# Kernel optimization log

Measured on AMD Instinct MI355X. Metric: run time of the kernel, lower is better.

## Reference

```python
import jax, jax.numpy as jnp
import numpy as np

N_NODES = 100000


def _graph_conv(x, W, b, src, dst, n_nodes):
    # dgl GraphConv, norm='both'. in_dim >= out_dim so weight is applied first.
    E = src.shape[0]
    ones = jnp.ones((E,), dtype=x.dtype)
    deg_out = jnp.clip(jax.ops.segment_sum(ones, src, num_segments=n_nodes), 1.0)
    deg_in = jnp.clip(jax.ops.segment_sum(ones, dst, num_segments=n_nodes), 1.0)
    h = x @ W                                  # [N, out]
    h = h * (deg_out ** -0.5)[:, None]          # src-side norm D_out^{-1/2}
    agg = jax.ops.segment_sum(h[src], dst, num_segments=n_nodes)  # SpMM
    agg = agg * (deg_in ** -0.5)[:, None]       # dst-side norm D_in^{-1/2}
    return agg + b


def setup_inputs() -> dict:
    key = jax.random.key(0)
    k1, k2, k3, k4, k5, k6, k7 = jax.random.split(key, 7)
    in_dim, hidden_dim, out_dim = 256, 128, 40
    E = 3200000
    h = jax.random.normal(k1, (N_NODES, in_dim), dtype=jnp.float32)
    src = jax.random.randint(k2, (E,), 0, N_NODES)
    dst = jax.random.randint(k3, (E,), 0, N_NODES)
    # Glorot-style init for GraphConv weights, zero bias (dgl default)
    W1 = jax.random.normal(k4, (in_dim, hidden_dim), dtype=jnp.float32) / np.sqrt(in_dim)
    b1 = jnp.zeros((hidden_dim,), dtype=jnp.float32)
    W2 = jax.random.normal(k5, (hidden_dim, out_dim), dtype=jnp.float32) / np.sqrt(hidden_dim)
    b2 = jnp.zeros((out_dim,), dtype=jnp.float32)
    return {"h": h, "W1": W1, "b1": b1, "W2": W2, "b2": b2, "src": src, "dst": dst}


def reference(h, W1, b1, W2, b2, src, dst):
    n = h.shape[0]
    # CRD: GraphConv -> relu (dropout is identity in eval)
    x = _graph_conv(h, W1, b1, src, dst, n)
    x = jax.nn.relu(x)
    # CLS: GraphConv -> log_softmax over classes
    x = _graph_conv(x, W2, b2, src, dst, n)
    return jax.nn.log_softmax(x, axis=1)
```

## Files before the change

kernel.cpp:

```cpp
#include <hip/hip_runtime.h>
#include <hip/hip_bf16.h>
#include <cstddef>
#include <cstdint>

#define IN_DIM 256
#define HID 128
#define OUT_DIM 40

#define CHUNK 8192
#define BIN_SHIFT 10
#define BIN_SIZE 1024
#define MAXB 128
#define GSPLIT 8

typedef __attribute__((ext_vector_type(8))) short short8;
typedef __attribute__((ext_vector_type(4))) float f32x4;
typedef __attribute__((ext_vector_type(2))) float f32x2;

__device__ inline short f2bf(float f) {
    __hip_bfloat16 b = __float2bfloat16(f);
    return __builtin_bit_cast(short, b);
}
__device__ inline float bf2f(unsigned short u) {
    unsigned int v = (unsigned int)u << 16;
    return __builtin_bit_cast(float, v);
}
__device__ inline int permf(int p) { return (p >> 3) + 16 * (p & 7); }

__global__ __launch_bounds__(256) void k_setup(const float* __restrict__ W1, const float* __restrict__ W2,
                                               const float* __restrict__ b1, short* __restrict__ Wg,
                                               short* __restrict__ Wg2, float* __restrict__ b1p,
                                               int* __restrict__ deg_in, int* __restrict__ deg_out, int Z) {
    int flat = blockIdx.x * 256 + threadIdx.x;
    if (flat < 8192) {
        int k = flat >> 5;
        int n0 = (flat & 31) * 4;
        float4 v = *(const float4*)(W1 + (size_t)k * HID + n0);
        int ks = k >> 5, quad = (k >> 3) & 3, j = k & 7;
        float vv[4] = {v.x, v.y, v.z, v.w};
#pragma unroll
        for (int e = 0; e < 4; ++e) {
            int n = n0 + e;
            int nt = n >> 4;
            int ln = (n & 15) | (quad << 4);
            Wg[(((nt * 8 + ks) * 64) + ln) * 8 + j] = f2bf(vv[e]);
        }
        return;
    }
    flat -= 8192;
    if (flat < 3 * 4 * 64 * 8) {
        int f = flat >> 9;
        int ln = (flat >> 3) & 63;
        int j = flat & 7;
        int nt = f >> 2, ks = f & 3;
        int q = ks * 32 + (ln >> 4) * 8 + j;
        int c = nt * 16 + (ln & 15);
        float v = (c < OUT_DIM) ? W2[(size_t)permf(q) * OUT_DIM + c] : 0.f;
        Wg2[flat] = f2bf(v);
        return;
    }
    flat -= 3 * 4 * 64 * 8;
    if (flat < HID) { b1p[flat] = b1[permf(flat)]; return; }
    flat -= HID;
    if (flat < Z) { *(int4*)(deg_in + flat * 4) = make_int4(0, 0, 0, 0); return; }
    flat -= Z;
    if (flat < Z) { *(int4*)(deg_out + flat * 4) = make_int4(0, 0, 0, 0); }
}

__global__ __launch_bounds__(256) void k_binscatter(const int* __restrict__ src, const int* __restrict__ dst,
                                                    uint32_t* __restrict__ stD, unsigned short* __restrict__ stS,
                                                    int* __restrict__ bboD, int* __restrict__ bboS,
                                                    int E, int NBINS) {
    __shared__ int hD[MAXB], hS[MAXB], cD[MAXB], cS[MAXB], sd[MAXB];
    int j = blockIdx.x, t = threadIdx.x;
    int base = j * CHUNK;
    int nE = min(CHUNK, E - base);
    int NB1 = NBINS + 1;
    for (int i = t; i < MAXB; i += 256) { hD[i] = 0; hS[i] = 0; }
    __syncthreads();
    for (int i = t; i < nE; i += 256) {
        atomicAdd(&hD[dst[base + i] >> BIN_SHIFT], 1);
        atomicAdd(&hS[src[base + i] >> BIN_SHIFT], 1);
    }
    __syncthreads();
    if (t < MAXB) sd[t] = hD[t];
    __syncthreads();
    for (int off = 1; off < MAXB; off <<= 1) {
        int x = 0;
        if (t < MAXB && t >= off) x = sd[t - off];
        __syncthreads();
        if (t < MAXB) sd[t] += x;
        __syncthreads();
    }
    if (t < MAXB) cD[t] = sd[t] - hD[t];
    if (t < NBINS) bboD[(size_t)j * NB1 + t] = sd[t] - hD[t];
    if (t == NBINS) bboD[(size_t)j * NB1 + NBINS] = nE;
    __syncthreads();
    if (t < MAXB) sd[t] = hS[t];
    __syncthreads();
    for (int off = 1; off < MAXB; off <<= 1) {
        int x = 0;
        if (t < MAXB && t >= off) x = sd[t - off];
        __syncthreads();
        if (t < MAXB) sd[t] += x;
        __syncthreads();
    }
    if (t < MAXB) cS[t] = sd[t] - hS[t];
    if (t < NBINS) bboS[(size_t)j * NB1 + t] = sd[t] - hS[t];
    if (t == NBINS) bboS[(size_t)j * NB1 + NBINS] = nE;
    __syncthreads();
    for (int i = t; i < nE; i += 256) {
        int s = src[base + i], d = dst[base + i];
        int pD = atomicAdd(&cD[d >> BIN_SHIFT], 1);
        stD[(size_t)base + pD] = ((uint32_t)(d & (BIN_SIZE - 1)) << 17) | (uint32_t)s;
        int pS = atomicAdd(&cS[s >> BIN_SHIFT], 1);
        stS[(size_t)base + pS] = (unsigned short)(s & (BIN_SIZE - 1));
    }
}

__global__ __launch_bounds__(256) void k_deg(const uint32_t* __restrict__ stD, const int* __restrict__ bboD,
                                             const unsigned short* __restrict__ stS, const int* __restrict__ bboS,
                                             int* __restrict__ deg_in, int* __restrict__ deg_out,
                                             int* __restrict__ hsave, int nchunk, int NBINS) {
    __shared__ int hist[BIN_SIZE];
    int b = blockIdx.x, g = blockIdx.y, t = threadIdx.x;
    int wv = t >> 6, lane = t & 63;
    int NB1 = NBINS + 1;
    for (int i = t; i < BIN_SIZE; i += 256) hist[i] = 0;
    __syncthreads();
    int base = b << BIN_SHIFT;
    if (blockIdx.z == 0) {
        for (int j = g * 4 + wv; j < nchunk; j += GSPLIT * 4) {
            int s = bboD[(size_t)j * NB1 + b], e = bboD[(size_t)j * NB1 + b + 1];
            const uint32_t* seg = stD + (size_t)j * CHUNK;
            for (int i = s + lane; i < e; i += 64)
                atomicAdd(&hist[seg[i] >> 17], 1);
        }
        __syncthreads();
        int* hp = hsave + ((size_t)(b * GSPLIT + g) << BIN_SHIFT);
        for (int i = t; i < BIN_SIZE; i += 256) {
            int v = hist[i];
            hp[i] = v;
            if (v) atomicAdd(&deg_in[base + i], v);
        }
    } else {
        for (int j = g * 4 + wv; j < nchunk; j += GSPLIT * 4) {
            int s = bboS[(size_t)j * NB1 + b], e = bboS[(size_t)j * NB1 + b + 1];
            const unsigned short* seg = stS + (size_t)j * CHUNK;
            for (int i = s + lane; i < e; i += 64)
                atomicAdd(&hist[seg[i]], 1);
        }
        __syncthreads();
        for (int i = t; i < BIN_SIZE; i += 256) {
            int v = hist[i];
            if (v) atomicAdd(&deg_out[base + i], v);
        }
    }
}

__global__ __launch_bounds__(256) void k_col(const uint32_t* __restrict__ stD, const int* __restrict__ bboD,
                                             const int* __restrict__ hsave, int* __restrict__ cursor,
                                             int* __restrict__ col, int N, int nchunk, int NBINS) {
    __shared__ int hist[BIN_SIZE];
    int b = blockIdx.x, g = blockIdx.y, t = threadIdx.x;
    int wv = t >> 6, lane = t & 63;
    int NB1 = NBINS + 1;
    int base = b << BIN_SHIFT;
    const int* hp = hsave + ((size_t)(b * GSPLIT + g) << BIN_SHIFT);
    for (int i = t; i < BIN_SIZE; i += 256) {
        int v = hp[i];
        hist[i] = v ? atomicAdd(&cursor[base + i], v) : 0;
    }
    __syncthreads();
    for (int j = g * 4 + wv; j < nchunk; j += GSPLIT * 4) {
        int s = bboD[(size_t)j * NB1 + b], e = bboD[(size_t)j * NB1 + b + 1];
        const uint32_t* seg = stD + (size_t)j * CHUNK;
        for (int i = s + lane; i < e; i += 64) {
            uint32_t v = seg[i];
            int pos = atomicAdd(&hist[v >> 17], 1);
            col[pos] = (int)(v & 0x1FFFFu);
        }
    }
}

__global__ __launch_bounds__(256) void k_scan1(const int* __restrict__ deg, int* __restrict__ out,
                                               int* __restrict__ bsum, float* __restrict__ rs_in, int n) {
    __shared__ int sd[256];
    int t = threadIdx.x, b = blockIdx.x;
    int base = b * 1024 + t * 4;
    int v0 = 0, v1 = 0, v2 = 0, v3 = 0;
    if (base + 0 < n) v0 = deg[base + 0];
    if (base + 1 < n) v1 = deg[base + 1];
    if (base + 2 < n) v2 = deg[base + 2];
    if (base + 3 < n) v3 = deg[base + 3];
    if (base + 0 < n) rs_in[base + 0] = rsqrtf((float)max(v0, 1));
    if (base + 1 < n) rs_in[base + 1] = rsqrtf((float)max(v1, 1));
    if (base + 2 < n) rs_in[base + 2] = rsqrtf((float)max(v2, 1));
    if (base + 3 < n) rs_in[base + 3] = rsqrtf((float)max(v3, 1));
    int ts = v0 + v1 + v2 + v3;
    sd[t] = ts;
    __syncthreads();
    for (int off = 1; off < 256; off <<= 1) {
        int x = 0;
        if (t >= off) x = sd[t - off];
        __syncthreads();
        sd[t] += x;
        __syncthreads();
    }
    int excl = sd[t] - ts;
    if (base + 0 < n) out[base + 0] = excl;
    if (base + 1 < n) out[base + 1] = excl + v0;
    if (base + 2 < n) out[base + 2] = excl + v0 + v1;
    if (base + 3 < n) out[base + 3] = excl + v0 + v1 + v2;
    if (t == 255) bsum[b] = sd[255];
}

__global__ __launch_bounds__(1024) void k_scan2(int* __restrict__ bsum, int nb) {
    __shared__ int sd[1024];
    int t = threadIdx.x;
    int v = (t < nb) ? bsum[t] : 0;
    sd[t] = v;
    __syncthreads();
    for (int off = 1; off < 1024; off <<= 1) {
        int x = 0;
        if (t >= off) x = sd[t - off];
        __syncthreads();
        sd[t] += x;
        __syncthreads();
    }
    if (t < nb) bsum[t] = sd[t] - v;
}

__global__ __launch_bounds__(256) void k_scan3(int* __restrict__ row_ptr, const int* __restrict__ bsum,
                                               int* __restrict__ cursor, const int* __restrict__ deg_out,
                                               float* __restrict__ rs_out, int n, int E) {
    int i = blockIdx.x * 256 + threadIdx.x;
    if (i < n) {
        int v = row_ptr[i] + bsum[i >> 10];
        row_ptr[i] = v;
        cursor[i] = v;
        rs_out[i] = rsqrtf((float)max(deg_out[i], 1));
    }
    if (i == 0) row_ptr[n] = E;
}

__global__ __launch_bounds__(256) void k_gemm1(const float* __restrict__ A, const short* __restrict__ Wg,
                                               const float* __restrict__ rs_out, uint32_t* __restrict__ h1f, int M) {
    __shared__ short As[64 * 264];
    int t = threadIdx.x;
    int lane = t & 63, wv = t >> 6;
    int block_row = blockIdx.x * 64;
#pragma unroll
    for (int i = 0; i < 16; ++i) {
        int u = t + i * 256;
        int row = u >> 6, kq = (u & 63) * 4;
        int gr = block_row + row;
        float4 v = {0.f, 0.f, 0.f, 0.f};
        if (gr < M) v = *(const float4*)(A + (size_t)gr * IN_DIM + kq);
        short4 sv = {f2bf(v.x), f2bf(v.y), f2bf(v.z), f2bf(v.w)};
        *(short4*)&As[row * 264 + kq] = sv;
    }
    __syncthreads();
    f32x4 acc[8] = {};
    int arow = (wv * 16 + (lane & 15)) * 264 + (lane >> 4) * 8;
#pragma unroll
    for (int ks = 0; ks < 8; ++ks) {
        short8 a = *(short8*)&As[arow + ks * 32];
#pragma unroll
        for (int nt = 0; nt < 8; ++nt) {
            short8 b = *(const short8*)&Wg[(((nt * 8 + ks) * 64) + lane) * 8];
            acc[nt] = __builtin_amdgcn_mfma_f32_16x16x32_bf16(a, b, acc[nt], 0, 0, 0);
        }
    }
    int quad = lane >> 4, cl = lane & 15;
#pragma unroll
    for (int r = 0; r < 4; ++r) {
        int gr = block_row + wv * 16 + quad * 4 + r;
        if (gr >= M) continue;
        float sc = rs_out[gr];
        int d0 = __builtin_amdgcn_cvt_pk_fp8_f32(acc[0][r] * sc, acc[1][r] * sc, 0, false);
        d0 = __builtin_amdgcn_cvt_pk_fp8_f32(acc[2][r] * sc, acc[3][r] * sc, d0, true);
        int d1 = __builtin_amdgcn_cvt_pk_fp8_f32(acc[4][r] * sc, acc[5][r] * sc, 0, false);
        d1 = __builtin_amdgcn_cvt_pk_fp8_f32(acc[6][r] * sc, acc[7][r] * sc, d1, true);
        uint2 dd = make_uint2((uint32_t)d0, (uint32_t)d1);
        *(uint2*)((char*)h1f + (size_t)gr * 128 + cl * 8) = dd;
    }
}

__global__ __launch_bounds__(256) void k_spmm1f(const char* __restrict__ h1c, const int* __restrict__ rp,
                                                const int* __restrict__ col, const float* __restrict__ rs_in,
                                                const float* __restrict__ rs_out, const float* __restrict__ b1p,
                                                const short* __restrict__ Wg2,
                                                uint32_t* __restrict__ h2f, int N) {
    __shared__ uint32_t x1s[16 * 64];
    __shared__ uint32_t hs2[48];
    int t = threadIdx.x;
    int wv = t >> 6, lane = t & 63;
    int grp = lane >> 4, ql = lane & 15;
    int w_base = blockIdx.x * 4;
    int w = w_base + wv;

    float4 blo = *(const float4*)&b1p[ql * 8];
    float4 bhi = *(const float4*)&b1p[ql * 8 + 4];

    if (w < N) {
        int s = rp[w], e = rp[w + 1];
        f32x2 a0 = {0.f, 0.f}, a1 = {0.f, 0.f}, a2 = {0.f, 0.f}, a3 = {0.f, 0.f};
        int qoff = ql << 3;
        int i = s;
        while (i < e) {
            int cnt = min(64, e - i);
            int cl = (lane < cnt) ? lane : cnt - 1;
            int rof = col[i + cl] << 7;
            int nfull = cnt & ~15;
            int it = 0;
            for (; it < nfull; it += 16) {
                int o0 = __shfl(rof, it + grp, 64) + qoff;
                int o1 = __shfl(rof, it + 4 + grp, 64) + qoff;
                int o2 = __shfl(rof, it + 8 + grp, 64) + qoff;
                int o3 = __shfl(rof, it + 12 + grp, 64) + qoff;
                uint2 u0 = *(const uint2*)(h1c + (uint32_t)o0);
                uint2 u1 = *(const uint2*)(h1c + (uint32_t)o1);
                uint2 u2 = *(const uint2*)(h1c + (uint32_t)o2);
                uint2 u3 = *(const uint2*)(h1c + (uint32_t)o3);
                a0 += __builtin_amdgcn_cvt_pk_f32_fp8(u0.x, false);
                a1 += __builtin_amdgcn_cvt_pk_f32_fp8(u0.x, true);
                a2 += __builtin_amdgcn_cvt_pk_f32_fp8(u0.y, false);
                a3 += __builtin_amdgcn_cvt_pk_f32_fp8(u0.y, true);
                a0 += __builtin_amdgcn_cvt_pk_f32_fp8(u1.x, false);
                a1 += __builtin_amdgcn_cvt_pk_f32_fp8(u1.x, true);
                a2 += __builtin_amdgcn_cvt_pk_f32_fp8(u1.y, false);
                a3 += __builtin_amdgcn_cvt_pk_f32_fp8(u1.y, true);
                a0 += __builtin_amdgcn_cvt_pk_f32_fp8(u2.x, false);
                a1 += __builtin_amdgcn_cvt_pk_f32_fp8(u2.x, true);
                a2 += __builtin_amdgcn_cvt_pk_f32_fp8(u2.y, false);
                a3 += __builtin_amdgcn_cvt_pk_f32_fp8(u2.y, true);
                a0 += __builtin_amdgcn_cvt_pk_f32_fp8(u3.x, false);
                a1 += __builtin_amdgcn_cvt_pk_f32_fp8(u3.x, true);
                a2 += __builtin_amdgcn_cvt_pk_f32_fp8(u3.y, false);
                a3 += __builtin_amdgcn_cvt_pk_f32_fp8(u3.y, true);
            }
            if (it < cnt) {
                int e0 = it + grp;
                int o0 = __shfl(rof, e0, 64) + qoff;
                int o1 = __shfl(rof, e0 + 4, 64) + qoff;
                int o2 = __shfl(rof, e0 + 8, 64) + qoff;
                int o3 = __shfl(rof, e0 + 12, 64) + qoff;
                float mv0 = (e0 < cnt) ? 1.f : 0.f;
                float mv1 = (e0 + 4 < cnt) ? 1.f : 0.f;
                float mv2 = (e0 + 8 < cnt) ? 1.f : 0.f;
                float mv3 = (e0 + 12 < cnt) ? 1.f : 0.f;
                f32x2 m0 = {mv0, mv0}, m1 = {mv1, mv1}, m2 = {mv2, mv2}, m3 = {mv3, mv3};
                uint2 u0 = *(const uint2*)(h1c + (uint32_t)o0);
                uint2 u1 = *(const uint2*)(h1c + (uint32_t)o1);
                uint2 u2 = *(const uint2*)(h1c + (uint32_t)o2);
                uint2 u3 = *(const uint2*)(h1c + (uint32_t)o3);
                a0 += __builtin_amdgcn_cvt_pk_f32_fp8(u0.x, false) * m0;
                a1 += __builtin_amdgcn_cvt_pk_f32_fp8(u0.x, true) * m0;
                a2 += __builtin_amdgcn_cvt_pk_f32_fp8(u0.y, false) * m0;
                a3 += __builtin_amdgcn_cvt_pk_f32_fp8(u0.y, true) * m0;
                a0 += __builtin_amdgcn_cvt_pk_f32_fp8(u1.x, false) * m1;
                a1 += __builtin_amdgcn_cvt_pk_f32_fp8(u1.x, true) * m1;
                a2 += __builtin_amdgcn_cvt_pk_f32_fp8(u1.y, false) * m1;
                a3 += __builtin_amdgcn_cvt_pk_f32_fp8(u1.y, true) * m1;
                a0 += __builtin_amdgcn_cvt_pk_f32_fp8(u2.x, false) * m2;
                a1 += __builtin_amdgcn_cvt_pk_f32_fp8(u2.x, true) * m2;
                a2 += __builtin_amdgcn_cvt_pk_f32_fp8(u2.y, false) * m2;
                a3 += __builtin_amdgcn_cvt_pk_f32_fp8(u2.y, true) * m2;
                a0 += __builtin_amdgcn_cvt_pk_f32_fp8(u3.x, false) * m3;
                a1 += __builtin_amdgcn_cvt_pk_f32_fp8(u3.x, true) * m3;
                a2 += __builtin_amdgcn_cvt_pk_f32_fp8(u3.y, false) * m3;
                a3 += __builtin_amdgcn_cvt_pk_f32_fp8(u3.y, true) * m3;
            }
            i += cnt;
        }
        float ac[8] = {a0.x, a0.y, a1.x, a1.y, a2.x, a2.y, a3.x, a3.y};
#pragma unroll
        for (int j = 0; j < 8; ++j) {
            ac[j] += __shfl_xor(ac[j], 16, 64);
            ac[j] += __shfl_xor(ac[j], 32, 64);
        }
        if (lane < 16) {
            float sc = rs_in[w];
            float f0, f1;
            uint32_t o0, o1, o2, o3;
            f0 = fmaxf(fmaf(ac[0], sc, blo.x), 0.f); f1 = fmaxf(fmaf(ac[1], sc, blo.y), 0.f);
            o0 = (uint32_t)(unsigned short)f2bf(f0) | ((uint32_t)(unsigned short)f2bf(f1) << 16);
            f0 = fmaxf(fmaf(ac[2], sc, blo.z), 0.f); f1 = fmaxf(fmaf(ac[3], sc, blo.w), 0.f);
            o1 = (uint32_t)(unsigned short)f2bf(f0) | ((uint32_t)(unsigned short)f2bf(f1) << 16);
            f0 = fmaxf(fmaf(ac[4], sc, bhi.x), 0.f); f1 = fmaxf(fmaf(ac[5], sc, bhi.y), 0.f);
            o2 = (uint32_t)(unsigned short)f2bf(f0) | ((uint32_t)(unsigned short)f2bf(f1) << 16);
            f0 = fmaxf(fmaf(ac[6], sc, bhi.z), 0.f); f1 = fmaxf(fmaf(ac[7], sc, bhi.w), 0.f);
            o3 = (uint32_t)(unsigned short)f2bf(f0) | ((uint32_t)(unsigned short)f2bf(f1) << 16);
            int woff = (wv * 256 + ql * 16) ^ ((wv & 7) << 4);
            *(uint4*)((char*)x1s + woff) = make_uint4(o0, o1, o2, o3);
        }
    }
    __syncthreads();
    int vr = min(4, N - w_base);
    if (wv < 3) {
        short8 wf0 = *(const short8*)&Wg2[((wv * 4 + 0) * 64 + lane) * 8];
        short8 wf1 = *(const short8*)&Wg2[((wv * 4 + 1) * 64 + lane) * 8];
        short8 wf2 = *(const short8*)&Wg2[((wv * 4 + 2) * 64 + lane) * 8];
        short8 wf3 = *(const short8*)&Wg2[((wv * 4 + 3) * 64 + lane) * 8];
        int row = lane & 15, kc = lane >> 4;
        int rbase = row * 256 + kc * 16;
        int swz = (row & 7) << 4;
        f32x4 c = {};
        c = __builtin_amdgcn_mfma_f32_16x16x32_bf16(*(short8*)((char*)x1s + ((rbase + 0) ^ swz)),   wf0, c, 0, 0, 0);
        c = __builtin_amdgcn_mfma_f32_16x16x32_bf16(*(short8*)((char*)x1s + ((rbase + 64) ^ swz)),  wf1, c, 0, 0, 0);
        c = __builtin_amdgcn_mfma_f32_16x16x32_bf16(*(short8*)((char*)x1s + ((rbase + 128) ^ swz)), wf2, c, 0, 0, 0);
        c = __builtin_amdgcn_mfma_f32_16x16x32_bf16(*(short8*)((char*)x1s + ((rbase + 192) ^ swz)), wf3, c, 0, 0, 0);
        int cc = wv * 16 + row;
        if (cc < OUT_DIM && kc == 0) {
            float s0 = rs_out[w_base + 0];
            float s1 = (vr > 1) ? rs_out[w_base + 1] : 0.f;
            float s2 = (vr > 2) ? rs_out[w_base + 2] : 0.f;
            float s3 = (vr > 3) ? rs_out[w_base + 3] : 0.f;
            int pk = __builtin_amdgcn_cvt_pk_fp8_f32(c[0] * s0, c[1] * s1, 0, false);
            pk = __builtin_amdgcn_cvt_pk_fp8_f32(c[2] * s2, c[3] * s3, pk, true);
            hs2[cc] = (uint32_t)pk;
        }
    }
    __syncthreads();
    if (t < 64) {
        int node = t >> 4, d = t & 15;
        uint32_t v = 0;
        if (d < 10) {
            int sh = node * 8;
            uint32_t b0 = (hs2[4 * d + 0] >> sh) & 0xffu;
            uint32_t b1 = (hs2[4 * d + 1] >> sh) & 0xffu;
            uint32_t b2 = (hs2[4 * d + 2] >> sh) & 0xffu;
            uint32_t b3 = (hs2[4 * d + 3] >> sh) & 0xffu;
            v = b0 | (b1 << 8) | (b2 << 16) | (b3 << 24);
        }
        if (node < vr) h2f[(size_t)(w_base + node) * 16 + d] = v;
    }
}

__global__ __launch_bounds__(256) void k_spmm2(const char* __restrict__ h2c, const int* __restrict__ rp,
                                               const int* __restrict__ col, const float* __restrict__ rs_in,
                                               const float* __restrict__ b2, float* __restrict__ out, int n) {
    int w = (blockIdx.x * 256 + threadIdx.x) >> 6;
    int lane = threadIdx.x & 63;
    if (w >= n) return;
    int grp = lane >> 3, fl = lane & 7;
    int qoff = fl << 3;
    int s = rp[w], e = rp[w + 1];
    f32x2 a0 = {0.f, 0.f}, a1 = {0.f, 0.f}, a2 = {0.f, 0.f}, a3 = {0.f, 0.f};
    int i = s;
    while (i < e) {
        int cnt = min(64, e - i);
        int cl = (lane < cnt) ? lane : cnt - 1;
        int rof = col[i + cl] << 6;
        int nfull = cnt & ~31;
        int it = 0;
        for (; it < nfull; it += 32) {
            int o0 = __shfl(rof, it + grp, 64) + qoff;
            int o1 = __shfl(rof, it + 8 + grp, 64) + qoff;
            int o2 = __shfl(rof, it + 16 + grp, 64) + qoff;
            int o3 = __shfl(rof, it + 24 + grp, 64) + qoff;
            uint2 u0 = *(const uint2*)(h2c + (uint32_t)o0);
            uint2 u1 = *(const uint2*)(h2c + (uint32_t)o1);
            uint2 u2 = *(const uint2*)(h2c + (uint32_t)o2);
            uint2 u3 = *(const uint2*)(h2c + (uint32_t)o3);
            a0 += __builtin_amdgcn_cvt_pk_f32_fp8(u0.x, false);
            a1 += __builtin_amdgcn_cvt_pk_f32_fp8(u0.x, true);
            a2 += __builtin_amdgcn_cvt_pk_f32_fp8(u0.y, false);
            a3 += __builtin_amdgcn_cvt_pk_f32_fp8(u0.y, true);
            a0 += __builtin_amdgcn_cvt_pk_f32_fp8(u1.x, false);
            a1 += __builtin_amdgcn_cvt_pk_f32_fp8(u1.x, true);
            a2 += __builtin_amdgcn_cvt_pk_f32_fp8(u1.y, false);
            a3 += __builtin_amdgcn_cvt_pk_f32_fp8(u1.y, true);
            a0 += __builtin_amdgcn_cvt_pk_f32_fp8(u2.x, false);
            a1 += __builtin_amdgcn_cvt_pk_f32_fp8(u2.x, true);
            a2 += __builtin_amdgcn_cvt_pk_f32_fp8(u2.y, false);
            a3 += __builtin_amdgcn_cvt_pk_f32_fp8(u2.y, true);
            a0 += __builtin_amdgcn_cvt_pk_f32_fp8(u3.x, false);
            a1 += __builtin_amdgcn_cvt_pk_f32_fp8(u3.x, true);
            a2 += __builtin_amdgcn_cvt_pk_f32_fp8(u3.y, false);
            a3 += __builtin_amdgcn_cvt_pk_f32_fp8(u3.y, true);
        }
        if (it < cnt) {
            int e0 = it + grp;
            int o0 = __shfl(rof, e0, 64) + qoff;
            int o1 = __shfl(rof, e0 + 8, 64) + qoff;
            int o2 = __shfl(rof, e0 + 16, 64) + qoff;
            int o3 = __shfl(rof, e0 + 24, 64) + qoff;
            float mv0 = (e0 < cnt) ? 1.f : 0.f;
            float mv1 = (e0 + 8 < cnt) ? 1.f : 0.f;
            float mv2 = (e0 + 16 < cnt) ? 1.f : 0.f;
            float mv3 = (e0 + 24 < cnt) ? 1.f : 0.f;
            f32x2 m0 = {mv0, mv0}, m1 = {mv1, mv1}, m2 = {mv2, mv2}, m3 = {mv3, mv3};
            uint2 u0 = *(const uint2*)(h2c + (uint32_t)o0);
            uint2 u1 = *(const uint2*)(h2c + (uint32_t)o1);
            uint2 u2 = *(const uint2*)(h2c + (uint32_t)o2);
            uint2 u3 = *(const uint2*)(h2c + (uint32_t)o3);
            a0 += __builtin_amdgcn_cvt_pk_f32_fp8(u0.x, false) * m0;
            a1 += __builtin_amdgcn_cvt_pk_f32_fp8(u0.x, true) * m0;
            a2 += __builtin_amdgcn_cvt_pk_f32_fp8(u0.y, false) * m0;
            a3 += __builtin_amdgcn_cvt_pk_f32_fp8(u0.y, true) * m0;
            a0 += __builtin_amdgcn_cvt_pk_f32_fp8(u1.x, false) * m1;
            a1 += __builtin_amdgcn_cvt_pk_f32_fp8(u1.x, true) * m1;
            a2 += __builtin_amdgcn_cvt_pk_f32_fp8(u1.y, false) * m1;
            a3 += __builtin_amdgcn_cvt_pk_f32_fp8(u1.y, true) * m1;
            a0 += __builtin_amdgcn_cvt_pk_f32_fp8(u2.x, false) * m2;
            a1 += __builtin_amdgcn_cvt_pk_f32_fp8(u2.x, true) * m2;
            a2 += __builtin_amdgcn_cvt_pk_f32_fp8(u2.y, false) * m2;
            a3 += __builtin_amdgcn_cvt_pk_f32_fp8(u2.y, true) * m2;
            a0 += __builtin_amdgcn_cvt_pk_f32_fp8(u3.x, false) * m3;
            a1 += __builtin_amdgcn_cvt_pk_f32_fp8(u3.x, true) * m3;
            a2 += __builtin_amdgcn_cvt_pk_f32_fp8(u3.y, false) * m3;
            a3 += __builtin_amdgcn_cvt_pk_f32_fp8(u3.y, true) * m3;
        }
        i += cnt;
    }
    float ac[8] = {a0.x, a0.y, a1.x, a1.y, a2.x, a2.y, a3.x, a3.y};
#pragma unroll
    for (int j = 0; j < 8; ++j) {
        ac[j] += __shfl_xor(ac[j], 8, 64);
        ac[j] += __shfl_xor(ac[j], 16, 64);
        ac[j] += __shfl_xor(ac[j], 32, 64);
    }
    bool act = lane < 5;
    float sc = rs_in[w];
    int bb = (fl < 5) ? fl * 8 : 0;
    float val[8];
#pragma unroll
    for (int j = 0; j < 8; ++j)
        val[j] = fmaf(ac[j], sc, b2[bb + j]);
    float pm = -INFINITY;
    if (act) {
        pm = val[0];
#pragma unroll
        for (int j = 1; j < 8; ++j) pm = fmaxf(pm, val[j]);
    }
    pm = fmaxf(pm, __shfl_xor(pm, 4, 8));
    pm = fmaxf(pm, __shfl_xor(pm, 2, 8));
    pm = fmaxf(pm, __shfl_xor(pm, 1, 8));
    float ex = 0.f;
    if (act) {
#pragma unroll
        for (int j = 0; j < 8; ++j) ex += expf(val[j] - pm);
    }
    ex += __shfl_xor(ex, 4, 8);
    ex += __shfl_xor(ex, 2, 8);
    ex += __shfl_xor(ex, 1, 8);
    if (act) {
        float l = pm + logf(ex);
        float4 o0 = {val[0] - l, val[1] - l, val[2] - l, val[3] - l};
        float4 o1 = {val[4] - l, val[5] - l, val[6] - l, val[7] - l};
        float* op = out + (size_t)w * OUT_DIM + lane * 8;
        *(float4*)op = o0;
        *(float4*)(op + 4) = o1;
    }
}


extern "C" void kernel_launch(void* const* d_in, const int* in_sizes, int n_in,
                              void* d_out, int out_size, void* d_ws, size_t ws_size,
                              hipStream_t stream) {
    const int N = in_sizes[0] / IN_DIM;
    const int E = in_sizes[5];
    const float* h  = (const float*)d_in[0];
    const float* W1 = (const float*)d_in[1];
    const float* b1 = (const float*)d_in[2];
    const float* W2 = (const float*)d_in[3];
    const float* b2 = (const float*)d_in[4];
    const int* src  = (const int*)d_in[5];
    const int* dst  = (const int*)d_in[6];
    float* out = (float*)d_out;

    const int NBINS  = (N + BIN_SIZE - 1) >> BIN_SHIFT;
    const int NCHUNK = (E + CHUNK - 1) / CHUNK;

    char* w = (char*)d_ws;
    size_t off = 0;
    auto alloc = [&](size_t bytes) -> void* {
        void* p = w + off;
        off += (bytes + 255) & ~(size_t)255;
        return p;
    };
    int* deg_in   = (int*)alloc((size_t)N * 4);
    int* deg_out  = (int*)alloc((size_t)N * 4);
    int* row_ptr  = (int*)alloc((size_t)(N + 1) * 4);
    int* cursor   = (int*)alloc((size_t)N * 4);
    int* bsum     = (int*)alloc(1024 * 4);
    float* rs_out = (float*)alloc((size_t)N * 4);
    float* rs_in  = (float*)alloc((size_t)N * 4);
    int* col      = (int*)alloc((size_t)E * 4);
    int* bboD     = (int*)alloc((size_t)NCHUNK * (NBINS + 1) * 4);
    int* bboS     = (int*)alloc((size_t)NCHUNK * (NBINS + 1) * 4);
    short* Wg     = (short*)alloc((size_t)8 * 8 * 64 * 8 * 2);
    short* Wg2    = (short*)alloc((size_t)3 * 4 * 64 * 8 * 2);
    float* b1p    = (float*)alloc((size_t)HID * 4);
    int* hsave    = (int*)alloc((size_t)NBINS * GSPLIT * BIN_SIZE * 4);
    size_t stD_bytes = (size_t)E * 4;  if ((size_t)N * HID > stD_bytes) stD_bytes = (size_t)N * HID;
    size_t stS_bytes = (size_t)E * 2;  if ((size_t)N * 64 > stS_bytes) stS_bytes = (size_t)N * 64;
    uint32_t* stD = (uint32_t*)alloc(stD_bytes);
    unsigned short* stS = (unsigned short*)alloc(stS_bytes);
    uint32_t* h1f = (uint32_t*)stD;
    uint32_t* h2f = (uint32_t*)stS;

    int gN = (N + 255) / 256;
    int NB = (N + 1023) / 1024;
    int Z = (N + 3) / 4;
    int setup_units = 8192 + 3 * 4 * 64 * 8 + HID + 2 * Z;
    int gsetup = (setup_units + 255) / 256;

    k_setup<<<gsetup, 256, 0, stream>>>(W1, W2, b1, Wg, Wg2, b1p, deg_in, deg_out, Z);
    k_binscatter<<<NCHUNK, 256, 0, stream>>>(src, dst, stD, stS, bboD, bboS, E, NBINS);
    k_deg<<<dim3(NBINS, GSPLIT, 2), 256, 0, stream>>>(stD, bboD, stS, bboS, deg_in, deg_out, hsave, NCHUNK, NBINS);
    k_scan1<<<NB, 256, 0, stream>>>(deg_in, row_ptr, bsum, rs_in, N);
    k_scan2<<<1, 1024, 0, stream>>>(bsum, NB);
    k_scan3<<<gN, 256, 0, stream>>>(row_ptr, bsum, cursor, deg_out, rs_out, N, E);
    k_col<<<dim3(NBINS, GSPLIT), 256, 0, stream>>>(stD, bboD, hsave, cursor, col, N, NCHUNK, NBINS);
    k_gemm1<<<(N + 63) / 64, 256, 0, stream>>>(h, Wg, rs_out, h1f, N);
    k_spmm1f<<<(N + 3) / 4, 256, 0, stream>>>((const char*)h1f, row_ptr, col, rs_in, rs_out, b1p, Wg2, h2f, N);
    k_spmm2<<<(N + 3) / 4, 256, 0, stream>>>((const char*)h2f, row_ptr, col, rs_in, b2, out, N);
}
```

Before: 463.1 us.

## Stage binned edges in shared memory, halve chunk size, fold block-sum scan into scan3

The bin-scatter kernel now writes binned edges into shared-memory staging arrays and then copies them to global memory with coalesced vector stores, replacing scattered global writes. The chunk size is halved to 4096 edges, which keeps the staging buffers within shared memory and doubles the number of blocks. The separate single-block scan2 launch is removed; each scan3 block redundantly scans up to 128 block sums itself. The trade-offs are more per-chunk offset metadata, which k_deg and k_col must then read, a redundant small scan in every scan3 block, and the assumption that NB is at most 128.

```diff
diff --git a/kernel.cpp b/kernel.cpp
--- a/kernel.cpp
+++ b/kernel.cpp
@@ -7,7 +7,7 @@
 #define HID 128
 #define OUT_DIM 40
 
-#define CHUNK 8192
+#define CHUNK 4096
 #define BIN_SHIFT 10
 #define BIN_SIZE 1024
 #define MAXB 128
@@ -71,7 +71,9 @@
                                                     uint32_t* __restrict__ stD, unsigned short* __restrict__ stS,
                                                     int* __restrict__ bboD, int* __restrict__ bboS,
                                                     int E, int NBINS) {
-    __shared__ int hD[MAXB], hS[MAXB], cD[MAXB], cS[MAXB], sd[MAXB];
+    __shared__ __align__(16) uint32_t sgD[CHUNK];
+    __shared__ __align__(16) unsigned short sgS[CHUNK];
+    __shared__ int hD[MAXB], hS[MAXB], sd[MAXB];
     int j = blockIdx.x, t = threadIdx.x;
     int base = j * CHUNK;
     int nE = min(CHUNK, E - base);
@@ -92,8 +94,12 @@
         if (t < MAXB) sd[t] += x;
         __syncthreads();
     }
-    if (t < MAXB) cD[t] = sd[t] - hD[t];
-    if (t < NBINS) bboD[(size_t)j * NB1 + t] = sd[t] - hD[t];
+    if (t < MAXB) {
+        int h = hD[t];
+        int c = sd[t] - h;
+        hD[t] = c;
+        if (t < NBINS) bboD[(size_t)j * NB1 + t] = c;
+    }
     if (t == NBINS) bboD[(size_t)j * NB1 + NBINS] = nE;
     __syncthreads();
     if (t < MAXB) sd[t] = hS[t];
@@ -105,17 +111,30 @@
         if (t < MAXB) sd[t] += x;
         __syncthreads();
     }
-    if (t < MAXB) cS[t] = sd[t] - hS[t];
-    if (t < NBINS) bboS[(size_t)j * NB1 + t] = sd[t] - hS[t];
+    if (t < MAXB) {
+        int h = hS[t];
+        int c = sd[t] - h;
+        hS[t] = c;
+        if (t < NBINS) bboS[(size_t)j * NB1 + t] = c;
+    }
     if (t == NBINS) bboS[(size_t)j * NB1 + NBINS] = nE;
     __syncthreads();
     for (int i = t; i < nE; i += 256) {
         int s = src[base + i], d = dst[base + i];
-        int pD = atomicAdd(&cD[d >> BIN_SHIFT], 1);
-        stD[(size_t)base + pD] = ((uint32_t)(d & (BIN_SIZE - 1)) << 17) | (uint32_t)s;
-        int pS = atomicAdd(&cS[s >> BIN_SHIFT], 1);
-        stS[(size_t)base + pS] = (unsigned short)(s & (BIN_SIZE - 1));
-    }
+        int pD = atomicAdd(&hD[d >> BIN_SHIFT], 1);
+        sgD[pD] = ((uint32_t)(d & (BIN_SIZE - 1)) << 17) | (uint32_t)s;
+        int pS = atomicAdd(&hS[s >> BIN_SHIFT], 1);
+        sgS[pS] = (unsigned short)(s & (BIN_SIZE - 1));
+    }
+    __syncthreads();
+    int nh = nE >> 1;
+    uint2* dD = (uint2*)(stD + base);
+    const uint2* sD = (const uint2*)sgD;
+    for (int i = t; i < nh; i += 256) dD[i] = sD[i];
+    uint32_t* dS = (uint32_t*)(stS + base);
+    const uint32_t* sS = (const uint32_t*)sgS;
+    for (int i = t; i < nh; i += 256) dS[i] = sS[i];
+    if ((nE & 1) && t == 0) { stD[base + nE - 1] = sgD[nE - 1]; stS[base + nE - 1] = sgS[nE - 1]; }
 }
 
 __global__ __launch_bounds__(256) void k_deg(const uint32_t* __restrict__ stD, const int* __restrict__ bboD,
@@ -215,28 +234,25 @@
     if (t == 255) bsum[b] = sd[255];
 }
 
-__global__ __launch_bounds__(1024) void k_scan2(int* __restrict__ bsum, int nb) {
-    __shared__ int sd[1024];
-    int t = threadIdx.x;
-    int v = (t < nb) ? bsum[t] : 0;
-    sd[t] = v;
-    __syncthreads();
-    for (int off = 1; off < 1024; off <<= 1) {
-        int x = 0;
-        if (t >= off) x = sd[t - off];
-        __syncthreads();
-        sd[t] += x;
-        __syncthreads();
-    }
-    if (t < nb) bsum[t] = sd[t] - v;
-}
-
 __global__ __launch_bounds__(256) void k_scan3(int* __restrict__ row_ptr, const int* __restrict__ bsum,
                                                int* __restrict__ cursor, const int* __restrict__ deg_out,
-                                               float* __restrict__ rs_out, int n, int E) {
+                                               float* __restrict__ rs_out, int n, int E, int NB) {
+    __shared__ int sb[128];
+    int t = threadIdx.x;
+    if (t < 128) sb[t] = (t < NB) ? bsum[t] : 0;
+    __syncthreads();
+    for (int off = 1; off < 128; off <<= 1) {
+        int x = 0;
+        if (t < 128 && t >= off) x = sb[t - off];
+        __syncthreads();
+        if (t < 128) sb[t] += x;
+        __syncthreads();
+    }
     int i = blockIdx.x * 256 + threadIdx.x;
     if (i < n) {
-        int v = row_ptr[i] + bsum[i >> 10];
+        int blk = i >> 10;
+        int add = (blk > 0) ? sb[blk - 1] : 0;
+        int v = row_ptr[i] + add;
         row_ptr[i] = v;
         cursor[i] = v;
         rs_out[i] = rsqrtf((float)max(deg_out[i], 1));
@@ -612,8 +628,7 @@
     k_binscatter<<<NCHUNK, 256, 0, stream>>>(src, dst, stD, stS, bboD, bboS, E, NBINS);
     k_deg<<<dim3(NBINS, GSPLIT, 2), 256, 0, stream>>>(stD, bboD, stS, bboS, deg_in, deg_out, hsave, NCHUNK, NBINS);
     k_scan1<<<NB, 256, 0, stream>>>(deg_in, row_ptr, bsum, rs_in, N);
-    k_scan2<<<1, 1024, 0, stream>>>(bsum, NB);
-    k_scan3<<<gN, 256, 0, stream>>>(row_ptr, bsum, cursor, deg_out, rs_out, N, E);
+    k_scan3<<<gN, 256, 0, stream>>>(row_ptr, bsum, cursor, deg_out, rs_out, N, E, NB);
     k_col<<<dim3(NBINS, GSPLIT), 256, 0, stream>>>(stD, bboD, hsave, cursor, col, N, NCHUNK, NBINS);
     k_gemm1<<<(N + 63) / 64, 256, 0, stream>>>(h, Wg, rs_out, h1f, N);
     k_spmm1f<<<(N + 3) / 4, 256, 0, stream>>>((const char*)h1f, row_ptr, col, rs_in, rs_out, b1p, Wg2, h2f, N);
```

Result: faster. 436.4 us (-5.8%).
